# Kernel optimization log

Measured on AMD Instinct MI355X. Metric: run time of the kernel, lower is better.

The kernel has to match this reference:

```python
import jax, jax.numpy as jnp
import numpy as np
from jax import lax

EPS = 1e-5
DIM = 96      # channels = dim
KS = 96       # kernel_size == H == W
GROUPS = 8
BATCH = 4
FFN_F = 2.66

# relative index table: emb[c, i, j] = rel[c, i - j + KS - 1]
_REL_IDX = (np.arange(KS)[:, None] - np.arange(KS)[None, :] + KS - 1).reshape(-1)


def _bn(x, g, b, ax):
    """BatchNorm (training-mode batch statistics) over all axes except `ax`."""
    axes = tuple(i for i in range(x.ndim) if i != ax)
    m = x.mean(axes, keepdims=True)
    v = x.var(axes, keepdims=True)
    sh = [1] * x.ndim
    sh[ax] = -1
    return (x - m) / jnp.sqrt(v + EPS) * g.reshape(sh) + b.reshape(sh)


def _ln(x, w, b):
    """WithBias LayerNorm over channel dim of NCHW (per-pixel over C)."""
    m = x.mean(1, keepdims=True)
    v = x.var(1, keepdims=True)
    return (x - m) / jnp.sqrt(v + EPS) * w[None, :, None, None] + b[None, :, None, None]


def _axial(x, wqkv, gq, bq, rel, gs, bs, go, bo, width):
    # x: (N, C, H, W)
    xp = x.transpose(0, 2, 1, 3) if width else x.transpose(0, 3, 1, 2)
    N, Wd, C, L = xp.shape
    gp = C // GROUPS  # group_planes
    xb = xp.reshape(N * Wd, C, L)
    qkv = _bn(jnp.einsum('oc,bcl->bol', wqkv, xb), gq, bq, 1)
    qkv = qkv.reshape(N * Wd, GROUPS, 2 * gp, L)
    q, k, v = qkv[:, :, :gp // 2], qkv[:, :, gp // 2:gp], qkv[:, :, gp:]
    emb = rel[:, _REL_IDX].reshape(2 * gp, L, L)
    qe, ke, ve = emb[:gp // 2], emb[gp // 2:gp], emb[gp:]
    qk = jnp.einsum('bgci,bgcj->bgij', q, k)
    qr = jnp.einsum('bgci,cij->bgij', q, qe)
    kr = jnp.einsum('bgci,cij->bgij', k, ke).transpose(0, 1, 3, 2)
    sim = _bn(jnp.concatenate([qk, qr, kr], 1), gs, bs, 1)
    sim = sim.reshape(N * Wd, 3, GROUPS, L, L).sum(1)
    sim = jax.nn.softmax(sim, axis=3)
    sv = jnp.einsum('bgij,bgcj->bgci', sim, v)
    sve = jnp.einsum('bgij,cij->bgci', sim, ve)
    out = _bn(jnp.concatenate([sv, sve], -1).reshape(N * Wd, 2 * C, L), go, bo, 1)
    out = out.reshape(N, Wd, C, 2, L).sum(3)
    return out.transpose(0, 2, 1, 3) if width else out.transpose(0, 2, 3, 1)


def _ffn(x, win, wdw, wout):
    h = jnp.einsum('oc,bchw->bohw', win, x)
    h = lax.conv_general_dilated(h, wdw, (1, 1), 'SAME',
                                 dimension_numbers=('NCHW', 'OIHW', 'NCHW'),
                                 feature_group_count=h.shape[1])
    x1, x2 = jnp.split(h, 2, axis=1)
    return jnp.einsum('oc,bchw->bohw', wout, jax.nn.gelu(x1, approximate=False) * x2)


def setup_inputs() -> dict:
    key = jax.random.key(0)
    ks = jax.random.split(key, 8)
    dim, gp = DIM, DIM // GROUPS
    hid = int(dim * FFN_F)
    f = jax.random.normal
    d = {'x': f(ks[0], (BATCH, dim, KS, KS), jnp.float32)}
    d['ln1_w'] = jnp.ones(dim); d['ln1_b'] = jnp.zeros(dim)
    for p, i in (('h_', 1), ('w_', 2)):
        k1, k2 = jax.random.split(ks[i])
        d[p + 'wqkv'] = f(k1, (2 * dim, dim), jnp.float32) * float(np.sqrt(1.0 / dim))
        d[p + 'gqkv'] = jnp.ones(2 * dim); d[p + 'bqkv'] = jnp.zeros(2 * dim)
        d[p + 'rel'] = f(k2, (2 * gp, 2 * KS - 1), jnp.float32) * float(np.sqrt(1.0 / gp))
        d[p + 'gsim'] = jnp.ones(3 * GROUPS); d[p + 'bsim'] = jnp.zeros(3 * GROUPS)
        d[p + 'gout'] = jnp.ones(2 * dim); d[p + 'bout'] = jnp.zeros(2 * dim)
    d['ln2_w'] = jnp.ones(dim); d['ln2_b'] = jnp.zeros(dim)
    d['ffn_win'] = f(ks[3], (2 * hid, dim), jnp.float32) * float(np.sqrt(1.0 / dim))
    d['ffn_wdw'] = f(ks[4], (2 * hid, 1, 3, 3), jnp.float32) * 0.1
    d['ffn_wout'] = f(ks[5], (dim, hid), jnp.float32) * float(np.sqrt(1.0 / hid))
    return d


def reference(x, ln1_w, ln1_b,
              h_wqkv, h_gqkv, h_bqkv, h_rel, h_gsim, h_bsim, h_gout, h_bout,
              w_wqkv, w_gqkv, w_bqkv, w_rel, w_gsim, w_bsim, w_gout, w_bout,
              ln2_w, ln2_b, ffn_win, ffn_wdw, ffn_wout):
    y = _ln(x, ln1_w, ln1_b)
    y = _axial(y, h_wqkv, h_gqkv, h_bqkv, h_rel, h_gsim, h_bsim, h_gout, h_bout, False)
    y = _axial(y, w_wqkv, w_gqkv, w_bqkv, w_rel, w_gsim, w_bsim, w_gout, w_bout, True)
    x = x + y
    x = x + _ffn(_ln(x, ln2_w, ln2_b), ffn_win, ffn_wdw, ffn_wout)
    return x
```

## Files before the change

kernel.cpp:

```cpp
#include <hip/hip_runtime.h>
#include <hip/hip_bf16.h>
#include <math.h>

using bf16 = __hip_bfloat16;

#define NB 4
#define C_ 96
#define NPIX 36864
#define IMG 9216
#define CH_ST 9216
#define N_ST 884736
#define HID 255
#define EPSF 1e-5f
#define TOT 3538944

__global__ __launch_bounds__(256) void ln_kernel(const float* __restrict__ X,
                                                 float* __restrict__ Y,
                                                 const float* __restrict__ w,
                                                 const float* __restrict__ b) {
  __shared__ float red[2][4][64];
  __shared__ float wb[192];
  int tid = threadIdx.x;
  if (tid < 192) wb[tid] = (tid < 96) ? w[tid] : b[tid - 96];
  int cq = tid >> 6, px = tid & 63;
  int pix = blockIdx.x * 64 + px;
  int n = pix / IMG, p = pix % IMG;
  const float* xp = X + (long)n * N_ST + (long)(cq * 24) * CH_ST + p;
  float xr[24];
  float s = 0.f, sq = 0.f;
  #pragma unroll
  for (int k = 0; k < 24; k++) {
    float v = xp[(long)k * CH_ST];
    xr[k] = v; s += v; sq += v * v;
  }
  red[0][cq][px] = s; red[1][cq][px] = sq;
  __syncthreads();
  float S  = red[0][0][px] + red[0][1][px] + red[0][2][px] + red[0][3][px];
  float SQ = red[1][0][px] + red[1][1][px] + red[1][2][px] + red[1][3][px];
  float m = S * (1.f / C_);
  float r = rsqrtf(fmaxf(SQ * (1.f / C_) - m * m, 0.f) + EPSF);
  float* yp = Y + (long)n * N_ST + (long)(cq * 24) * CH_ST + p;
  #pragma unroll
  for (int k = 0; k < 24; k++)
    yp[(long)k * CH_ST] = (xr[k] - m) * r * wb[cq * 24 + k] + wb[96 + cq * 24 + k];
}

__global__ void trans_kernel(const float* __restrict__ Y0, float* __restrict__ Y0C) {
  __shared__ float T[32][33];
  int nc = blockIdx.z; int n = nc / C_, c = nc % C_;
  int h0 = blockIdx.x * 32, w0 = blockIdx.y * 32;
  int tx = threadIdx.x, ty = threadIdx.y;
  const float* src = Y0 + (long)n * N_ST + (long)c * CH_ST;
  for (int r = 0; r < 4; r++)
    T[ty + 8 * r][tx] = src[(h0 + ty + 8 * r) * 96 + w0 + tx];
  __syncthreads();
  float* dst = Y0C + (long)c * NPIX + (long)n * IMG;
  for (int r = 0; r < 4; r++)
    dst[(w0 + ty + 8 * r) * 96 + h0 + tx] = T[tx][ty + 8 * r];
}

template<int TM, int TN, int EPI>
__global__ __launch_bounds__(256) void gemm_kernel(
    const float* __restrict__ A, const float* __restrict__ B,
    float* __restrict__ Cout, int M, int K, int NperZ,
    long bCstride, long bZstride, int batch,
    const float* __restrict__ X1, float* __restrict__ OutF) {
  constexpr int NT = TN / 16;
  constexpr int RT = TM / 16;
  __shared__ float As[32][TM];
  __shared__ float Bs[32][TN + 4];
  const int tx = threadIdx.x, ty = threadIdx.y;
  const int tid = ty * 16 + tx;
  const int m0 = blockIdx.y * TM;
  const int q0 = blockIdx.x * TN;
  const int z  = blockIdx.z;
  const float* Bz = B + (long)z * bZstride;
  float acc[RT][NT];
  #pragma unroll
  for (int a = 0; a < RT; a++)
    #pragma unroll
    for (int b = 0; b < NT; b++) acc[a][b] = 0.f;

  for (int kk = 0; kk < K; kk += 32) {
    #pragma unroll
    for (int it = 0; it < (32 * TM) / 256; it++) {
      int i = tid + it * 256;
      int c = i / TM, r = i % TM;
      int mm = m0 + r, kc = kk + c;
      As[c][r] = (mm < M && kc < K) ? A[(long)mm * K + kc] : 0.f;
    }
    #pragma unroll
    for (int it = 0; it < (32 * TN) / 256; it++) {
      int i = tid + it * 256;
      int c = i / TN, q = i % TN;
      int kc = kk + c;
      Bs[c][q] = (kc < K) ? Bz[(long)kc * bCstride + q0 + q] : 0.f;
    }
    __syncthreads();
    for (int kc = 0; kc < 32; kc++) {
      float av[RT];
      if constexpr (RT % 4 == 0) {
        #pragma unroll
        for (int u = 0; u < RT / 4; u++) {
          float4 a4 = *(const float4*)&As[kc][ty * RT + 4 * u];
          av[4 * u] = a4.x; av[4 * u + 1] = a4.y; av[4 * u + 2] = a4.z; av[4 * u + 3] = a4.w;
        }
      } else {
        #pragma unroll
        for (int u = 0; u < RT / 2; u++) {
          float2 a2 = *(const float2*)&As[kc][ty * RT + 2 * u];
          av[2 * u] = a2.x; av[2 * u + 1] = a2.y;
        }
      }
      float bv[NT];
      #pragma unroll
      for (int v4 = 0; v4 < NT / 4; v4++) {
        float4 b4 = *(const float4*)&Bs[kc][v4 * 64 + tx * 4];
        bv[v4 * 4] = b4.x; bv[v4 * 4 + 1] = b4.y; bv[v4 * 4 + 2] = b4.z; bv[v4 * 4 + 3] = b4.w;
      }
      #pragma unroll
      for (int a = 0; a < RT; a++)
        #pragma unroll
        for (int b = 0; b < NT; b++)
          acc[a][b] = fmaf(av[a], bv[b], acc[a][b]);
    }
    __syncthreads();
  }
  const long oStride = (long)NperZ * gridDim.z;
  if (EPI == 0) {
    #pragma unroll
    for (int a = 0; a < RT; a++) {
      int mm = m0 + ty * RT + a;
      if (mm < M) {
        float* dst = Cout + (long)mm * oStride + (long)z * NperZ + q0;
        #pragma unroll
        for (int v4 = 0; v4 < NT / 4; v4++)
          *(float4*)(dst + v4 * 64 + tx * 4) =
              make_float4(acc[a][v4 * 4], acc[a][v4 * 4 + 1],
                          acc[a][v4 * 4 + 2], acc[a][v4 * 4 + 3]);
      }
    }
  } else {
    #pragma unroll
    for (int a = 0; a < RT; a++) {
      int mm = m0 + ty * RT + a;
      if (mm < M) {
        #pragma unroll
        for (int v4 = 0; v4 < NT / 4; v4++) {
          int Q = q0 + v4 * 64 + tx * 4;
          int n = batch + z + Q / IMG, p = Q % IMG;
          long base = (long)n * N_ST + (long)mm * CH_ST + p;
          #pragma unroll
          for (int b = 0; b < 4; b++)
            OutF[base + b] = acc[a][v4 * 4 + b] + X1[base + b];
        }
      }
    }
  }
}

__global__ __launch_bounds__(1024) void rowstat_kernel(const float* __restrict__ D,
                                                       const float* __restrict__ g,
                                                       const float* __restrict__ b,
                                                       float2* __restrict__ aff) {
  int o = blockIdx.x;
  const float4* p = (const float4*)(D + (long)o * NPIX);
  float s = 0.f, sq = 0.f;
  for (int i = threadIdx.x; i < NPIX / 4; i += 1024) {
    float4 v = p[i];
    s  += v.x + v.y + v.z + v.w;
    sq += v.x * v.x + v.y * v.y + v.z * v.z + v.w * v.w;
  }
  for (int off = 32; off; off >>= 1) { s += __shfl_down(s, off); sq += __shfl_down(sq, off); }
  __shared__ float ss[16], ssq[16];
  int wv = threadIdx.x >> 6, lane = threadIdx.x & 63;
  if (lane == 0) { ss[wv] = s; ssq[wv] = sq; }
  __syncthreads();
  if (threadIdx.x == 0) {
    float S = 0.f, SQ = 0.f;
    #pragma unroll
    for (int i = 0; i < 16; i++) { S += ss[i]; SQ += ssq[i]; }
    float m = S / (float)NPIX;
    float var = fmaxf(SQ / (float)NPIX - m * m, 0.f);
    float sc = g[o] * rsqrtf(var + EPSF);
    aff[o] = make_float2(sc, b[o] - m * sc);
  }
}

__global__ void relstat_kernel(const float* __restrict__ relp, float* __restrict__ tbl) {
  int i = threadIdx.x;
  if (i >= 96) return;
  int side = blockIdx.x / 27, row = blockIdx.x % 27;
  const float* base = relp + side * 6 * 191;
  float* T = tbl + side * 27 * 96;
  if (row < 6) {
    float s = 0.f;
    for (int d = 0; d < 96; d++) s += base[row * 191 + i + d];
    T[row * 96 + i] = s;
  } else {
    int p = row - 6, c = 0;
    while (p >= 6 - c) { p -= 6 - c; c++; }
    int c2 = c + p;
    float s = 0.f;
    for (int d = 0; d < 96; d++) s += base[c * 191 + i + d] * base[c2 * 191 + i + d];
    T[576 + (row - 6) * 96 + i] = s;
  }
}

__global__ __launch_bounds__(256) void simstat2_kernel(const float* __restrict__ QKV,
                                                       const float2* __restrict__ aff,
                                                       const float* __restrict__ tbl,
                                                       float* __restrict__ stats) {
  int g = blockIdx.x & 7, chunk = blockIdx.x >> 3;
  int bbg = threadIdx.x >> 5, lane = threadIdx.x & 31;
  int bb = chunk * 8 + bbg;
  const float* Aq = tbl;
  const float* Wq = tbl + 6 * 96;
  const float* Ak = tbl + 27 * 96;
  const float* Wk = tbl + 27 * 96 + 6 * 96;
  float Sq[6] = {}, Sk[6] = {}, Gq[21] = {}, Gk[21] = {};
  float lq = 0.f, lsq = 0.f, lk = 0.f, lsk = 0.f;
  #pragma unroll
  for (int ii = 0; ii < 3; ii++) {
    int i = lane + 32 * ii;
    float qv[6], kv[6];
    #pragma unroll
    for (int c = 0; c < 6; c++) {
      int oq = g * 24 + c, ok = g * 24 + 6 + c;
      float2 a = aff[oq], b2 = aff[ok];
      qv[c] = QKV[(long)oq * NPIX + bb * 96 + i] * a.x + a.y;
      kv[c] = QKV[(long)ok * NPIX + bb * 96 + i] * b2.x + b2.y;
      Sq[c] += qv[c]; Sk[c] += kv[c];
      lq = fmaf(qv[c], Aq[c * 96 + i], lq);
      lk = fmaf(kv[c], Ak[c * 96 + i], lk);
    }
    int p = 0;
    #pragma unroll
    for (int c = 0; c < 6; c++)
      #pragma unroll
      for (int c2 = c; c2 < 6; c2++, p++) {
        float f = (c == c2) ? 1.f : 2.f;
        float pq = qv[c] * qv[c2], pk = kv[c] * kv[c2];
        Gq[p] += pq; Gk[p] += pk;
        lsq = fmaf(pq * f, Wq[p * 96 + i], lsq);
        lsk = fmaf(pk * f, Wk[p * 96 + i], lsk);
      }
  }
  #pragma unroll
  for (int off = 16; off; off >>= 1) {
    #pragma unroll
    for (int c = 0; c < 6; c++) { Sq[c] += __shfl_down(Sq[c], off, 32); Sk[c] += __shfl_down(Sk[c], off, 32); }
    #pragma unroll
    for (int p = 0; p < 21; p++) { Gq[p] += __shfl_down(Gq[p], off, 32); Gk[p] += __shfl_down(Gk[p], off, 32); }
    lq += __shfl_down(lq, off, 32);  lsq += __shfl_down(lsq, off, 32);
    lk += __shfl_down(lk, off, 32);  lsk += __shfl_down(lsk, off, 32);
  }
  __shared__ float red[6];
  if (threadIdx.x < 6) red[threadIdx.x] = 0.f;
  __syncthreads();
  if (lane == 0) {
    float sqk = 0.f, sqk2 = 0.f;
    #pragma unroll
    for (int c = 0; c < 6; c++) sqk += Sq[c] * Sk[c];
    int p = 0;
    #pragma unroll
    for (int c = 0; c < 6; c++)
      #pragma unroll
      for (int c2 = c; c2 < 6; c2++, p++)
        sqk2 += ((c == c2) ? 1.f : 2.f) * Gq[p] * Gk[p];
    atomicAdd(&red[0], sqk); atomicAdd(&red[3], sqk2);
    atomicAdd(&red[1], lq);  atomicAdd(&red[4], lsq);
    atomicAdd(&red[2], lk);  atomicAdd(&red[5], lsk);
  }
  __syncthreads();
  if (threadIdx.x < 3) {
    atomicAdd(&stats[(threadIdx.x * 8 + g) * 2 + 0], red[threadIdx.x]);
    atomicAdd(&stats[(threadIdx.x * 8 + g) * 2 + 1], red[threadIdx.x + 3]);
  }
}

__global__ void simfin_kernel(const float* __restrict__ stats,
                              const float* __restrict__ gsim,
                              float* __restrict__ scale) {
  int t = threadIdx.x;
  if (t < 24) {
    float cnt = 384.f * 9216.f;
    float m = stats[t * 2] / cnt;
    float var = fmaxf(stats[t * 2 + 1] / cnt - m * m, 0.f);
    scale[t] = gsim[t] * rsqrtf(var + EPSF);
  }
}

__global__ __launch_bounds__(256) void attn_kernel(const float* __restrict__ QKV,
                                                   const float2* __restrict__ aff,
                                                   const float* __restrict__ relp,
                                                   const float* __restrict__ sscale,
                                                   float* __restrict__ OutPre) {
  int blk = blockIdx.x;
  int bb = blk >> 3, g = blk & 7;
  __shared__ float qF[6][96];
  __shared__ float kF[6][96];
  __shared__ float vF[12][96];
  __shared__ float rl[24 * 191];
  __shared__ float P[32][100];
  int tid = threadIdx.x;
  float s0 = sscale[g], s1 = sscale[8 + g], s2 = sscale[16 + g];
  for (int i = tid; i < 288; i += 256) {
    int half = i / 144, r = i % 144;
    int c = r / 24, qd = r % 24;
    int o = g * 24 + half * 6 + c;
    float2 a = aff[o];
    float4 v = *(const float4*)(QKV + (long)o * NPIX + bb * 96 + qd * 4);
    float4 w = make_float4(v.x * a.x + a.y, v.y * a.x + a.y,
                           v.z * a.x + a.y, v.w * a.x + a.y);
    if (half == 0) *(float4*)&qF[c][qd * 4] = w;
    else           *(float4*)&kF[c][qd * 4] = w;
  }
  for (int i = tid; i < 288; i += 256) {
    int c = i / 24, qd = i % 24;
    int o = g * 24 + 12 + c;
    float2 a = aff[o];
    float4 v = *(const float4*)(QKV + (long)o * NPIX + bb * 96 + qd * 4);
    *(float4*)&vF[c][qd * 4] = make_float4(v.x * a.x + a.y, v.y * a.x + a.y,
                                           v.z * a.x + a.y, v.w * a.x + a.y);
  }
  for (int i = tid; i < 1146; i += 256) {
    int e = i * 4;
    float4 v = *(const float4*)(relp + e);
    float4 w;
    w.x = v.x * ((e + 0) < 1146 ? s1 : (e + 0) < 2292 ? s2 : 1.f);
    w.y = v.y * ((e + 1) < 1146 ? s1 : (e + 1) < 2292 ? s2 : 1.f);
    w.z = v.z * ((e + 2) < 1146 ? s1 : (e + 2) < 2292 ? s2 : 1.f);
    w.w = v.w * ((e + 3) < 1146 ? s1 : (e + 3) < 2292 ? s2 : 1.f);
    *(float4*)&rl[e] = w;
  }
  __syncthreads();
  int hw = tid >> 5, l32 = tid & 31;
  float kreg[6][3];
  #pragma unroll
  for (int c = 0; c < 6; c++)
    #pragma unroll
    for (int j = 0; j < 3; j++) kreg[c][j] = kF[c][l32 * 3 + j];
  for (int iq = 0; iq < 3; iq++) {
    int i0 = iq * 32;
    {
      int til = hw * 4;
      int ti = i0 + til;
      int tj = l32 * 3;
      int d0 = ti - tj + 93;
      int e0 = tj - ti + 92;
      float ap[4][3] = {};
      #pragma unroll
      for (int c = 0; c < 6; c++) {
        float4 q4 = *(const float4*)&qF[c][ti];
        float qv[4] = {q4.x, q4.y, q4.z, q4.w};
        float kv0[3], rq[6], rk[6];
        #pragma unroll
        for (int j = 0; j < 3; j++) kv0[j] = s0 * kreg[c][j];
        #pragma unroll
        for (int u = 0; u < 6; u++) { rq[u] = rl[c * 191 + d0 + u]; rk[u] = rl[(6 + c) * 191 + e0 + u]; }
        #pragma unroll
        for (int ii = 0; ii < 4; ii++)
          #pragma unroll
          for (int jj = 0; jj < 3; jj++) {
            ap[ii][jj] = fmaf(qv[ii], kv0[jj], ap[ii][jj]);
            ap[ii][jj] = fmaf(qv[ii], rq[ii - jj + 2], ap[ii][jj]);
            ap[ii][jj] = fmaf(kreg[c][jj], rk[jj - ii + 3], ap[ii][jj]);
          }
      }
      #pragma unroll
      for (int ii = 0; ii < 4; ii++)
        #pragma unroll
        for (int jj = 0; jj < 3; jj++)
          P[til + ii][l32 * 3 + jj] = ap[ii][jj];
    }
    __syncthreads();
    {
      int wv = tid >> 6, rloc = (tid >> 3) & 7, l8 = tid & 7;
      int r = wv * 8 + rloc;
      float* Pr = &P[r][l8 * 12];
      float4 v0 = *(const float4*)(Pr);
      float4 v1 = *(const float4*)(Pr + 4);
      float4 v2 = *(const float4*)(Pr + 8);
      float mx = fmaxf(fmaxf(fmaxf(v0.x, v0.y), fmaxf(v0.z, v0.w)),
                 fmaxf(fmaxf(fmaxf(v1.x, v1.y), fmaxf(v1.z, v1.w)),
                       fmaxf(fmaxf(v2.x, v2.y), fmaxf(v2.z, v2.w))));
      #pragma unroll
      for (int off = 4; off; off >>= 1) mx = fmaxf(mx, __shfl_xor(mx, off, 8));
      v0 = make_float4(__expf(v0.x - mx), __expf(v0.y - mx), __expf(v0.z - mx), __expf(v0.w - mx));
      v1 = make_float4(__expf(v1.x - mx), __expf(v1.y - mx), __expf(v1.z - mx), __expf(v1.w - mx));
      v2 = make_float4(__expf(v2.x - mx), __expf(v2.y - mx), __expf(v2.z - mx), __expf(v2.w - mx));
      float s = v0.x + v0.y + v0.z + v0.w + v1.x + v1.y + v1.z + v1.w
              + v2.x + v2.y + v2.z + v2.w;
      #pragma unroll
      for (int off = 4; off; off >>= 1) s += __shfl_xor(s, off, 8);
      *(float4*)(Pr)     = v0;
      *(float4*)(Pr + 4) = v1;
      *(float4*)(Pr + 8) = v2;
      if (l8 == 0) P[r][96] = 1.f / s;
    }
    __syncthreads();
    {
      int orr0 = hw * 3;
      float acc3[3] = {};
      for (int jq = 0; jq < 24; jq++) {
        int j0 = jq * 4;
        float4 pv = *(const float4*)&P[l32][j0];
        #pragma unroll
        for (int u = 0; u < 3; u++) {
          int orr = orr0 + u, cc = orr >> 1;
          if ((orr & 1) == 0) {
            float4 vv = *(const float4*)&vF[cc][j0];
            acc3[u] += pv.x * vv.x + pv.y * vv.y + pv.z * vv.z + pv.w * vv.w;
          } else {
            const float* rv = &rl[(12 + cc) * 191];
            int bse = (i0 + l32) - j0 + 92;
            float f0 = rv[bse], f1 = rv[bse + 1], f2 = rv[bse + 2], f3 = rv[bse + 3];
            acc3[u] += pv.w * f0 + pv.z * f1 + pv.y * f2 + pv.x * f3;
          }
        }
      }
      float ri = P[l32][96];
      #pragma unroll
      for (int u = 0; u < 3; u++)
        OutPre[(long)(g * 24 + orr0 + u) * NPIX + bb * 96 + i0 + l32] = acc3[u] * ri;
    }
    __syncthreads();
  }
}

__global__ void apply1_kernel(const float* __restrict__ OutPre,
                              const float2* __restrict__ aff,
                              float* __restrict__ Y1) {
  __shared__ float T[32][33];
  int z = blockIdx.z; int n = z / C_, cf = z % C_;
  int h0 = blockIdx.x * 32, w0 = blockIdx.y * 32;
  int tx = threadIdx.x, ty = threadIdx.y;
  float2 a0 = aff[2 * cf], a1 = aff[2 * cf + 1];
  const float* r0 = OutPre + (long)(2 * cf) * NPIX + (long)n * IMG;
  const float* r1 = OutPre + (long)(2 * cf + 1) * NPIX + (long)n * IMG;
  for (int r = 0; r < 4; r++) {
    int w = w0 + ty + 8 * r;
    int idx = w * 96 + h0 + tx;
    T[ty + 8 * r][tx] = (r0[idx] * a0.x + a0.y) + (r1[idx] * a1.x + a1.y);
  }
  __syncthreads();
  float* dst = Y1 + (long)n * N_ST + (long)cf * CH_ST;
  for (int r = 0; r < 4; r++)
    dst[(h0 + ty + 8 * r) * 96 + w0 + tx] = T[tx][ty + 8 * r];
}

__global__ __launch_bounds__(256) void apply2_kernel(const float* __restrict__ OutPre,
                                                     const float2* __restrict__ aff,
                                                     const float* __restrict__ X,
                                                     float* __restrict__ X1out) {
  int idx = blockIdx.x * 256 + threadIdx.x;
  if (idx >= TOT) return;
  int n = idx / N_ST;
  int rem = idx % N_ST;
  int cf = rem / CH_ST;
  int p = rem % CH_ST;
  long off = (long)n * IMG + p;
  float2 a0 = aff[2 * cf], a1 = aff[2 * cf + 1];
  float v = OutPre[(long)(2 * cf) * NPIX + off] * a0.x + a0.y
          + OutPre[(long)(2 * cf + 1) * NPIX + off] * a1.x + a1.y
          + X[idx];
  X1out[idx] = v;
}

__global__ __launch_bounds__(256) void dwglu_kernel(const float* __restrict__ H,
                                                    const float* __restrict__ Wdw,
                                                    float* __restrict__ Gout) {
  int idx = blockIdx.x * 256 + threadIdx.x;
  if (idx >= HID * IMG) return;
  int c = idx / IMG;
  int p = idx % IMG, y = p / 96, x = p % 96;
  const float* h1 = H + (long)c * IMG;
  const float* h2 = H + (long)(c + HID) * IMG;
  const float* w1 = Wdw + c * 9;
  const float* w2 = Wdw + (c + HID) * 9;
  float acc1 = 0.f, acc2 = 0.f;
  #pragma unroll
  for (int dy = -1; dy <= 1; dy++) {
    int yy = y + dy; if (yy < 0 || yy >= 96) continue;
    #pragma unroll
    for (int dx = -1; dx <= 1; dx++) {
      int xx = x + dx; if (xx < 0 || xx >= 96) continue;
      int wi = (dy + 1) * 3 + dx + 1;
      acc1 = fmaf(h1[yy * 96 + xx], w1[wi], acc1);
      acc2 = fmaf(h2[yy * 96 + xx], w2[wi], acc2);
    }
  }
  float ge = 0.5f * acc1 * (1.f + erff(acc1 * 0.70710678118654752f));
  Gout[idx] = ge * acc2;
}

extern "C" void kernel_launch(void* const* d_in, const int* in_sizes, int n_in,
                              void* d_out, int out_size, void* d_ws, size_t ws_size,
                              hipStream_t stream) {
  const float* x       = (const float*)d_in[0];
  const float* ln1w    = (const float*)d_in[1];
  const float* ln1b    = (const float*)d_in[2];
  const float* h_wqkv  = (const float*)d_in[3];
  const float* h_gqkv  = (const float*)d_in[4];
  const float* h_bqkv  = (const float*)d_in[5];
  const float* h_rel   = (const float*)d_in[6];
  const float* h_gsim  = (const float*)d_in[7];
  const float* h_gout  = (const float*)d_in[9];
  const float* h_bout  = (const float*)d_in[10];
  const float* w_wqkv  = (const float*)d_in[11];
  const float* w_gqkv  = (const float*)d_in[12];
  const float* w_bqkv  = (const float*)d_in[13];
  const float* w_rel   = (const float*)d_in[14];
  const float* w_gsim  = (const float*)d_in[15];
  const float* w_gout  = (const float*)d_in[17];
  const float* w_bout  = (const float*)d_in[18];
  const float* ln2w    = (const float*)d_in[19];
  const float* ln2b    = (const float*)d_in[20];
  const float* ffn_win = (const float*)d_in[21];
  const float* ffn_wdw = (const float*)d_in[22];
  const float* ffn_wout= (const float*)d_in[23];
  float* out = (float*)d_out;

  float* ws = (float*)d_ws;
  float* P = ws;
  float* Q = ws + 3538944;
  float* R = ws + 7077888;
  float* S = ws + 14155776;
  float* Gall = R;
  float* Hbuf = ws + 16478208;
  float* stats = ws + 21233664;
  const size_t need_bytes = (21233664ull + 8192ull) * 4ull;
  if (ws_size < need_bytes) return;

  float2* qkv_aff = (float2*)stats;
  float2* out_aff = (float2*)(stats + 384);
  float*  sim_st  = stats + 768;
  float*  sim_sc  = stats + 864;
  float*  tbl     = stats + 1024;

  hipMemsetAsync(sim_st, 0, 96 * sizeof(float), stream);

  dim3 b256(256), b1616(16, 16), b328(32, 8);

  ln_kernel<<<576, b256, 0, stream>>>(x, P, ln1w, ln1b);
  trans_kernel<<<dim3(3, 3, 384), b328, 0, stream>>>(P, Q);

  gemm_kernel<96, 128, 0><<<dim3(288, 2, 1), b1616, 0, stream>>>(h_wqkv, Q, R,
      192, 96, 36864, 36864L, 0L, 0, nullptr, nullptr);
  rowstat_kernel<<<192, 1024, 0, stream>>>(R, h_gqkv, h_bqkv, qkv_aff);
  relstat_kernel<<<54, 96, 0, stream>>>(h_rel, tbl);
  simstat2_kernel<<<384, b256, 0, stream>>>(R, qkv_aff, tbl, sim_st);
  simfin_kernel<<<1, 32, 0, stream>>>(sim_st, h_gsim, sim_sc);
  attn_kernel<<<3072, b256, 0, stream>>>(R, qkv_aff, h_rel, sim_sc, S);
  rowstat_kernel<<<192, 1024, 0, stream>>>(S, h_gout, h_bout, out_aff);
  apply1_kernel<<<dim3(3, 3, 384), b328, 0, stream>>>(S, out_aff, P);

  gemm_kernel<96, 128, 0><<<dim3(72, 2, 4), b1616, 0, stream>>>(w_wqkv, P, R,
      192, 96, 9216, 9216L, 884736L, 0, nullptr, nullptr);
  rowstat_kernel<<<192, 1024, 0, stream>>>(R, w_gqkv, w_bqkv, qkv_aff);
  relstat_kernel<<<54, 96, 0, stream>>>(w_rel, tbl);
  simstat2_kernel<<<384, b256, 0, stream>>>(R, qkv_aff, tbl, sim_st + 48);
  simfin_kernel<<<1, 32, 0, stream>>>(sim_st + 48, w_gsim, sim_sc + 24);
  attn_kernel<<<3072, b256, 0, stream>>>(R, qkv_aff, w_rel, sim_sc + 24, S);
  rowstat_kernel<<<192, 1024, 0, stream>>>(S, w_gout, w_bout, out_aff);
  apply2_kernel<<<13824, b256, 0, stream>>>(S, out_aff, x, P);

  ln_kernel<<<576, b256, 0, stream>>>(P, Q, ln2w, ln2b);
  for (int n = 0; n < NB; n++) {
    gemm_kernel<128, 64, 0><<<dim3(144, 4, 1), b1616, 0, stream>>>(ffn_win, Q + (long)n * N_ST, Hbuf,
        510, 96, 9216, 9216L, 0L, 0, nullptr, nullptr);
    dwglu_kernel<<<9180, b256, 0, stream>>>(Hbuf, ffn_wdw, Gall + (long)n * 2350080);
  }
  gemm_kernel<96, 64, 1><<<dim3(144, 1, 4), b1616, 0, stream>>>(ffn_wout, Gall, nullptr,
      96, 255, 9216, 9216L, 2350080L, 0, P, out);
}
```

Measured before the change: 907.8 us.

## Fuse residual apply with LayerNorm2 and batch FFN input GEMM and dwconv

Merges the second axial output affine, the residual add and the LN2 LayerNorm into one kernel that keeps 24 channels per thread in registers, so the separate elementwise pass and its extra read/write of the full activation go away. When the workspace is large enough, the four per-image FFN input GEMM and depthwise-GLU launches become one batched GEMM and one dwconv kernel over a bigger hidden buffer, cutting launch count and giving each launch more parallelism. The batched path depends on the workspace size and otherwise falls back to the old per-image loop. It also uses more register pressure in the fused LN kernel.

```diff
diff --git a/kernel.cpp b/kernel.cpp
--- a/kernel.cpp
+++ b/kernel.cpp
@@ -450,22 +450,49 @@
     dst[(h0 + ty + 8 * r) * 96 + w0 + tx] = T[tx][ty + 8 * r];
 }
 
-__global__ __launch_bounds__(256) void apply2_kernel(const float* __restrict__ OutPre,
-                                                     const float2* __restrict__ aff,
-                                                     const float* __restrict__ X,
-                                                     float* __restrict__ X1out) {
-  int idx = blockIdx.x * 256 + threadIdx.x;
-  if (idx >= TOT) return;
-  int n = idx / N_ST;
-  int rem = idx % N_ST;
-  int cf = rem / CH_ST;
-  int p = rem % CH_ST;
-  long off = (long)n * IMG + p;
-  float2 a0 = aff[2 * cf], a1 = aff[2 * cf + 1];
-  float v = OutPre[(long)(2 * cf) * NPIX + off] * a0.x + a0.y
-          + OutPre[(long)(2 * cf + 1) * NPIX + off] * a1.x + a1.y
-          + X[idx];
-  X1out[idx] = v;
+__global__ __launch_bounds__(256) void apl2_kernel(const float* __restrict__ OutPre,
+                                                   const float2* __restrict__ aff,
+                                                   const float* __restrict__ X,
+                                                   const float* __restrict__ w,
+                                                   const float* __restrict__ b,
+                                                   float* __restrict__ X1out,
+                                                   float* __restrict__ Yln) {
+  __shared__ float red[2][4][64];
+  __shared__ float2 affs[192];
+  __shared__ float wb[192];
+  int tid = threadIdx.x;
+  if (tid < 192) { affs[tid] = aff[tid]; wb[tid] = (tid < 96) ? w[tid] : b[tid - 96]; }
+  __syncthreads();
+  int cq = tid >> 6, px = tid & 63;
+  int pix = blockIdx.x * 64 + px;
+  int n = pix / IMG, p = pix % IMG;
+  const float* o0p = OutPre + (long)n * IMG + p;
+  const float* xp = X + (long)n * N_ST + (long)(cq * 24) * CH_ST + p;
+  float vr[24];
+  float s = 0.f, sq = 0.f;
+  #pragma unroll
+  for (int k = 0; k < 24; k++) {
+    int c = cq * 24 + k;
+    float2 a0 = affs[2 * c], a1 = affs[2 * c + 1];
+    float o0 = o0p[(long)(2 * c) * NPIX];
+    float o1 = o0p[(long)(2 * c + 1) * NPIX];
+    float v = o0 * a0.x + a0.y + o1 * a1.x + a1.y + xp[(long)k * CH_ST];
+    vr[k] = v; s += v; sq += v * v;
+  }
+  red[0][cq][px] = s; red[1][cq][px] = sq;
+  __syncthreads();
+  float S  = red[0][0][px] + red[0][1][px] + red[0][2][px] + red[0][3][px];
+  float SQ = red[1][0][px] + red[1][1][px] + red[1][2][px] + red[1][3][px];
+  float m = S * (1.f / C_);
+  float r = rsqrtf(fmaxf(SQ * (1.f / C_) - m * m, 0.f) + EPSF);
+  float* x1p = X1out + (long)n * N_ST + (long)(cq * 24) * CH_ST + p;
+  float* yp  = Yln   + (long)n * N_ST + (long)(cq * 24) * CH_ST + p;
+  #pragma unroll
+  for (int k = 0; k < 24; k++) {
+    x1p[(long)k * CH_ST] = vr[k];
+    int c = cq * 24 + k;
+    yp[(long)k * CH_ST] = (vr[k] - m) * r * wb[c] + wb[96 + c];
+  }
 }
 
 __global__ __launch_bounds__(256) void dwglu_kernel(const float* __restrict__ H,
@@ -493,6 +520,35 @@
   }
   float ge = 0.5f * acc1 * (1.f + erff(acc1 * 0.70710678118654752f));
   Gout[idx] = ge * acc2;
+}
+
+__global__ __launch_bounds__(256) void dwglu4_kernel(const float* __restrict__ H,
+                                                     const float* __restrict__ Wdw,
+                                                     float* __restrict__ Gout) {
+  int idx = blockIdx.x * 256 + threadIdx.x;
+  if (idx >= HID * IMG * NB) return;
+  int c = idx / (IMG * NB);
+  int rem = idx % (IMG * NB);
+  int nb = rem / IMG;
+  int p = rem % IMG, y = p / 96, x = p % 96;
+  const float* h1 = H + (long)c * (IMG * NB) + (long)nb * IMG;
+  const float* h2 = H + (long)(c + HID) * (IMG * NB) + (long)nb * IMG;
+  const float* w1 = Wdw + c * 9;
+  const float* w2 = Wdw + (c + HID) * 9;
+  float acc1 = 0.f, acc2 = 0.f;
+  #pragma unroll
+  for (int dy = -1; dy <= 1; dy++) {
+    int yy = y + dy; if (yy < 0 || yy >= 96) continue;
+    #pragma unroll
+    for (int dx = -1; dx <= 1; dx++) {
+      int xx = x + dx; if (xx < 0 || xx >= 96) continue;
+      int wi = (dy + 1) * 3 + dx + 1;
+      acc1 = fmaf(h1[yy * 96 + xx], w1[wi], acc1);
+      acc2 = fmaf(h2[yy * 96 + xx], w2[wi], acc2);
+    }
+  }
+  float ge = 0.5f * acc1 * (1.f + erff(acc1 * 0.70710678118654752f));
+  Gout[(long)nb * 2350080 + (long)c * IMG + p] = ge * acc2;
 }
 
 extern "C" void kernel_launch(void* const* d_in, const int* in_sizes, int n_in,
@@ -529,9 +585,11 @@
   float* S = ws + 14155776;
   float* Gall = R;
   float* Hbuf = ws + 16478208;
-  float* stats = ws + 21233664;
-  const size_t need_bytes = (21233664ull + 8192ull) * 4ull;
-  if (ws_size < need_bytes) return;
+  const size_t base_need = (21233664ull + 8192ull) * 4ull;
+  const size_t big_need  = (35278848ull + 8192ull) * 4ull;
+  if (ws_size < base_need) return;
+  const bool batched = (ws_size >= big_need);
+  float* stats = batched ? (ws + 35278848) : (ws + 21233664);
 
   float2* qkv_aff = (float2*)stats;
   float2* out_aff = (float2*)(stats + 384);
@@ -564,13 +622,18 @@
   simfin_kernel<<<1, 32, 0, stream>>>(sim_st + 48, w_gsim, sim_sc + 24);
   attn_kernel<<<3072, b256, 0, stream>>>(R, qkv_aff, w_rel, sim_sc + 24, S);
   rowstat_kernel<<<192, 1024, 0, stream>>>(S, w_gout, w_bout, out_aff);
-  apply2_kernel<<<13824, b256, 0, stream>>>(S, out_aff, x, P);
-
-  ln_kernel<<<576, b256, 0, stream>>>(P, Q, ln2w, ln2b);
-  for (int n = 0; n < NB; n++) {
-    gemm_kernel<128, 64, 0><<<dim3(144, 4, 1), b1616, 0, stream>>>(ffn_win, Q + (long)n * N_ST, Hbuf,
-        510, 96, 9216, 9216L, 0L, 0, nullptr, nullptr);
-    dwglu_kernel<<<9180, b256, 0, stream>>>(Hbuf, ffn_wdw, Gall + (long)n * 2350080);
+  apl2_kernel<<<576, b256, 0, stream>>>(S, out_aff, x, ln2w, ln2b, P, Q);
+
+  if (batched) {
+    gemm_kernel<128, 64, 0><<<dim3(144, 4, 4), b1616, 0, stream>>>(ffn_win, Q, Hbuf,
+        510, 96, 9216, 9216L, 884736L, 0, nullptr, nullptr);
+    dwglu4_kernel<<<36720, b256, 0, stream>>>(Hbuf, ffn_wdw, Gall);
+  } else {
+    for (int n = 0; n < NB; n++) {
+      gemm_kernel<128, 64, 0><<<dim3(144, 4, 1), b1616, 0, stream>>>(ffn_win, Q + (long)n * N_ST, Hbuf,
+          510, 96, 9216, 9216L, 0L, 0, nullptr, nullptr);
+      dwglu_kernel<<<9180, b256, 0, stream>>>(Hbuf, ffn_wdw, Gall + (long)n * 2350080);
+    }
   }
   gemm_kernel<96, 64, 1><<<dim3(144, 1, 4), b1616, 0, stream>>>(ffn_wout, Gall, nullptr,
       96, 255, 9216, 9216L, 2350080L, 0, P, out);
```

Result: faster. 852.9 us, median of 3 (-6.0%).
